# Kernel optimization log

Hardware: AMD Instinct MI355X
Metric: run time of the kernel (lower is better)

## Reference

```python
import jax, jax.numpy as jnp
import numpy as np

D_K = 64
D_MODEL = 1024
N_HEADS = 16


def setup_inputs() -> dict:
    key = jax.random.key(0)
    ks = jax.random.split(key, 9)
    B, S = 2, 2048
    scale = 1.0 / np.sqrt(D_MODEL)
    inp = {
        "x": jax.random.normal(ks[0], (B, S, D_MODEL), dtype=jnp.float32),
        "w_q": jax.random.normal(ks[1], (D_MODEL, N_HEADS * D_K), dtype=jnp.float32) * scale,
        "b_q": jnp.zeros((N_HEADS * D_K,), dtype=jnp.float32),
        "w_k": jax.random.normal(ks[2], (D_MODEL, N_HEADS * D_K), dtype=jnp.float32) * scale,
        "b_k": jnp.zeros((N_HEADS * D_K,), dtype=jnp.float32),
        "w_v": jax.random.normal(ks[3], (D_MODEL, N_HEADS * D_K), dtype=jnp.float32) * scale,
        "b_v": jnp.zeros((N_HEADS * D_K,), dtype=jnp.float32),
        "w_o": jax.random.normal(ks[4], (N_HEADS * D_K, D_MODEL), dtype=jnp.float32) * scale,
        "b_o": jnp.zeros((D_MODEL,), dtype=jnp.float32),
    }
    return inp


def reference(x, w_q, b_q, w_k, b_k, w_v, b_v, w_o, b_o):
    B, S, _ = x.shape
    H, Dk = N_HEADS, D_K

    def split_heads(m):  # [B,S,H*Dk] -> [B,H,S,Dk]
        return m.reshape(B, S, H, Dk).transpose(0, 2, 1, 3)

    Q = split_heads(x @ w_q + b_q)
    K = split_heads(x @ w_k + b_k)
    V = split_heads(x @ w_v + b_v)

    scores = jnp.einsum("bhsd,bhtd->bhst", Q, K) / jnp.sqrt(jnp.float32(Dk))
    probs = jax.nn.softmax(scores, axis=-1)
    attn = jnp.einsum("bhst,bhtd->bhsd", probs, V)  # [B,H,S,Dk]
    attn = attn.transpose(0, 2, 1, 3).reshape(B, S, H * Dk)
    return attn @ w_o + b_o
```

## Files before the change

### kernel.cpp

```cpp
#include <hip/hip_runtime.h>
#include <math.h>

#define D_MODELc 1024
#define N_HEADSc 16
#define D_Kc     64
#define B_SZc    2
#define S_LENc   2048
#define NTOKc    (B_SZc * S_LENc)

using half8  = __attribute__((ext_vector_type(8))) _Float16;
using half4  = __attribute__((ext_vector_type(4))) _Float16;
using fp16x2 = __attribute__((ext_vector_type(2))) __fp16;
using float4v = __attribute__((ext_vector_type(4))) float;

__global__ __launch_bounds__(256) void cvt_all(
    const float* __restrict__ x,
    const float* __restrict__ W0, const float* __restrict__ W1,
    const float* __restrict__ W2, const float* __restrict__ W3,
    _Float16* __restrict__ wout, _Float16* __restrict__ xout)
{
    __shared__ float T[32][33];
    const int z = blockIdx.z;
    const int t = threadIdx.x;

    if (z == 4) {
        const int bid = blockIdx.y * 32 + blockIdx.x;
        #pragma unroll
        for (int c = 0; c < 2; ++c) {
            const int i = bid * 512 + c * 256 + t;
            float4v a = ((const float4v*)x)[2 * i];
            float4v b = ((const float4v*)x)[2 * i + 1];
            half8 h;
            h[0] = (_Float16)a[0]; h[1] = (_Float16)a[1];
            h[2] = (_Float16)a[2]; h[3] = (_Float16)a[3];
            h[4] = (_Float16)b[0]; h[5] = (_Float16)b[1];
            h[6] = (_Float16)b[2]; h[7] = (_Float16)b[3];
            ((half8*)xout)[i] = h;
        }
        return;
    }

    const float* W = (z == 0) ? W0 : (z == 1) ? W1 : (z == 2) ? W2 : W3;
    _Float16* O = wout + (size_t)z * 1024 * 1024;

    const int k0 = blockIdx.x * 32;
    const int n0 = blockIdx.y * 32;
    {
        const int r = t >> 3, c4 = (t & 7) * 4;
        float4v v = *(const float4v*)(W + (size_t)(k0 + r) * 1024 + n0 + c4);
        T[r][c4 + 0] = v[0]; T[r][c4 + 1] = v[1];
        T[r][c4 + 2] = v[2]; T[r][c4 + 3] = v[3];
    }
    __syncthreads();
    {
        const int rn = t >> 3, ck4 = (t & 7) * 4;
        half4 h;
        h[0] = (_Float16)T[ck4 + 0][rn];
        h[1] = (_Float16)T[ck4 + 1][rn];
        h[2] = (_Float16)T[ck4 + 2][rn];
        h[3] = (_Float16)T[ck4 + 3][rn];
        *(half4*)(O + (size_t)(n0 + rn) * 1024 + k0 + ck4) = h;
    }
}

template <int MODE>
__global__ __launch_bounds__(256) void gemm_f16(
    const _Float16* __restrict__ A, const _Float16* __restrict__ BtAll,
    const float* __restrict__ bias0, const float* __restrict__ bias1,
    const float* __restrict__ bias2, void* __restrict__ Cout)
{
    __shared__ _Float16 Als[128 * 32];
    __shared__ _Float16 Bls[128 * 32];

    constexpr int K = 1024;
    const int tid = threadIdx.x;
    const int m0  = blockIdx.x * 128;
    const int n0  = blockIdx.y * 128;
    const int z   = blockIdx.z;

    const _Float16* Bt  = BtAll + (size_t)z * 1024 * 1024;
    const float* bias   = (z == 0) ? bias0 : (z == 1) ? bias1 : bias2;
    const float qscale  = (MODE == 1 && z == 0) ? 0.18033688011112042f : 1.0f;

    const int wave = tid >> 6, lane = tid & 63;
    const int wr = wave >> 1, wc = wave & 1;
    const int quad = lane >> 4, l16 = lane & 15;

    float4v acc[4][4];
    #pragma unroll
    for (int i = 0; i < 4; ++i)
        #pragma unroll
        for (int j = 0; j < 4; ++j)
            acc[i][j] = (float4v){0.f, 0.f, 0.f, 0.f};

    for (int k0 = 0; k0 < K; k0 += 32) {
        #pragma unroll
        for (int c = 0; c < 2; ++c) {
            const int i   = c * 256 + tid;
            const int row = i >> 2, kc = i & 3;
            const _Float16* ga = A  + (size_t)(m0 + row) * K + k0 + kc * 8;
            const _Float16* gb = Bt + (size_t)(n0 + row) * K + k0 + kc * 8;
            __builtin_amdgcn_global_load_lds(
                (const __attribute__((address_space(1))) void*)ga,
                (__attribute__((address_space(3))) void*)(Als + i * 8), 16, 0, 0);
            __builtin_amdgcn_global_load_lds(
                (const __attribute__((address_space(1))) void*)gb,
                (__attribute__((address_space(3))) void*)(Bls + i * 8), 16, 0, 0);
        }
        __syncthreads();

        half8 af[4], bf[4];
        #pragma unroll
        for (int i = 0; i < 4; ++i) {
            const int r = wr * 64 + i * 16 + l16;
            af[i] = *(const half8*)(Als + r * 32 + quad * 8);
        }
        #pragma unroll
        for (int j = 0; j < 4; ++j) {
            const int cidx = wc * 64 + j * 16 + l16;
            bf[j] = *(const half8*)(Bls + cidx * 32 + quad * 8);
        }
        #pragma unroll
        for (int i = 0; i < 4; ++i)
            #pragma unroll
            for (int j = 0; j < 4; ++j)
                acc[i][j] = __builtin_amdgcn_mfma_f32_16x16x32_f16(
                    af[i], bf[j], acc[i][j], 0, 0, 0);
        __syncthreads();
    }

    if constexpr (MODE == 0) {
        #pragma unroll
        for (int i = 0; i < 4; ++i) {
            const int rbase = m0 + wr * 64 + i * 16 + quad * 4;
            #pragma unroll
            for (int j = 0; j < 4; ++j) {
                const int col = n0 + wc * 64 + j * 16 + l16;
                const float bv = bias[col];
                #pragma unroll
                for (int r = 0; r < 4; ++r)
                    ((float*)Cout)[(size_t)(rbase + r) * 1024 + col] =
                        acc[i][j][r] + bv;
            }
        }
    } else {
        if (z != 2) {
            #pragma unroll
            for (int i = 0; i < 4; ++i) {
                const int rbase = m0 + wr * 64 + i * 16 + quad * 4;
                #pragma unroll
                for (int j = 0; j < 4; ++j) {
                    const int col = n0 + wc * 64 + j * 16 + l16;
                    const float bv = bias[col];
                    #pragma unroll
                    for (int r = 0; r < 4; ++r) {
                        const float v = (acc[i][j][r] + bv) * qscale;
                        const int n = rbase + r;
                        const int b = n >> 11, s = n & 2047;
                        const int h = col >> 6, d = col & 63;
                        _Float16* C = (_Float16*)Cout + (size_t)z * NTOKc * D_MODELc;
                        C[(((size_t)(b * N_HEADSc + h)) * S_LENc + s) * D_Kc + d] =
                            (_Float16)v;
                    }
                }
            }
        } else {
            #pragma unroll
            for (int i = 0; i < 4; ++i) {
                const int rbase = m0 + wr * 64 + i * 16 + quad * 4;
                const int b = rbase >> 11, s0 = rbase & 2047;
                #pragma unroll
                for (int j = 0; j < 4; ++j) {
                    const int col = n0 + wc * 64 + j * 16 + l16;
                    const float bv = bias[col];
                    const int h = col >> 6, d = col & 63;
                    half4 hv;
                    #pragma unroll
                    for (int r = 0; r < 4; ++r)
                        hv[r] = (_Float16)(acc[i][j][r] + bv);
                    _Float16* C = (_Float16*)Cout + (size_t)2 * NTOKc * D_MODELc;
                    *(half4*)(C + (((size_t)(b * N_HEADSc + h)) * D_Kc + d) *
                              S_LENc + s0) = hv;
                }
            }
        }
    }
}

__global__ __launch_bounds__(256) void attn_mfma(
    const _Float16* __restrict__ Qb, const _Float16* __restrict__ Kb,
    const _Float16* __restrict__ Vtg, _Float16* __restrict__ Op,
    float* __restrict__ Lp)
{
    constexpr int PS = 72;
    __shared__ _Float16 Ks[64 * PS];
    __shared__ _Float16 Vt[64 * PS];
    __shared__ _Float16 Ps[128 * PS];

    const int tid  = threadIdx.x;
    const int wv   = tid >> 6;
    const int lane = tid & 63;
    const int quad = lane >> 4;
    const int l16  = lane & 15;

    const int q0 = blockIdx.x * 128;
    const int bh = blockIdx.y;
    const int sp = blockIdx.z;
    const int kb = sp * (S_LENc / 2);

    const _Float16* Qsl = Qb  + (size_t)bh * S_LENc * D_Kc;
    const _Float16* Ksl = Kb  + (size_t)bh * S_LENc * D_Kc;
    const _Float16* Vsl = Vtg + (size_t)bh * S_LENc * D_Kc;

    half8 aq[2][2];
    #pragma unroll
    for (int qf = 0; qf < 2; ++qf) {
        const int row = q0 + wv * 32 + qf * 16 + l16;
        aq[qf][0] = *(const half8*)(Qsl + (size_t)row * 64 + quad * 8);
        aq[qf][1] = *(const half8*)(Qsl + (size_t)row * 64 + 32 + quad * 8);
    }

    float4v O[2][4];
    #pragma unroll
    for (int qf = 0; qf < 2; ++qf)
        #pragma unroll
        for (int nt = 0; nt < 4; ++nt)
            O[qf][nt] = (float4v){0.f, 0.f, 0.f, 0.f};
    float lr[2] = {0.f, 0.f};

    const int sr = tid >> 2;
    const int sg = (tid & 3) * 16;

    for (int t0 = kb; t0 < kb + S_LENc / 2; t0 += 64) {
        half8 k0 = *(const half8*)(Ksl + (size_t)(t0 + sr) * 64 + sg);
        half8 k1 = *(const half8*)(Ksl + (size_t)(t0 + sr) * 64 + sg + 8);
        half8 v0 = *(const half8*)(Vsl + (size_t)sr * S_LENc + t0 + sg);
        half8 v1 = *(const half8*)(Vsl + (size_t)sr * S_LENc + t0 + sg + 8);
        __syncthreads();
        *(half8*)(Ks + sr * PS + sg)     = k0;
        *(half8*)(Ks + sr * PS + sg + 8) = k1;
        *(half8*)(Vt + sr * PS + sg)     = v0;
        *(half8*)(Vt + sr * PS + sg + 8) = v1;
        __syncthreads();

        half8 kf[4][2];
        #pragma unroll
        for (int nt = 0; nt < 4; ++nt) {
            kf[nt][0] = *(const half8*)(Ks + (nt * 16 + l16) * PS + quad * 8);
            kf[nt][1] = *(const half8*)(Ks + (nt * 16 + l16) * PS + 32 + quad * 8);
        }

        #pragma unroll
        for (int qf = 0; qf < 2; ++qf) {
            float4v st[4];
            #pragma unroll
            for (int nt = 0; nt < 4; ++nt) {
                st[nt] = __builtin_amdgcn_mfma_f32_16x16x32_f16(
                    kf[nt][0], aq[qf][0], (float4v){0.f, 0.f, 0.f, 0.f}, 0, 0, 0);
                st[nt] = __builtin_amdgcn_mfma_f32_16x16x32_f16(
                    kf[nt][1], aq[qf][1], st[nt], 0, 0, 0);
            }
            float ls = 0.f;
            #pragma unroll
            for (int nt = 0; nt < 4; ++nt) {
                const float p0 = __builtin_amdgcn_exp2f(fminf(st[nt][0], 15.5f));
                const float p1 = __builtin_amdgcn_exp2f(fminf(st[nt][1], 15.5f));
                const float p2 = __builtin_amdgcn_exp2f(fminf(st[nt][2], 15.5f));
                const float p3 = __builtin_amdgcn_exp2f(fminf(st[nt][3], 15.5f));
                ls += (p0 + p1) + (p2 + p3);
                union { fp16x2 h2[2]; half4 h4; } u;
                u.h2[0] = __builtin_amdgcn_cvt_pkrtz(p0, p1);
                u.h2[1] = __builtin_amdgcn_cvt_pkrtz(p2, p3);
                *(half4*)(Ps + (wv * 32 + qf * 16 + l16) * PS +
                          nt * 16 + quad * 4) = u.h4;
            }
            lr[qf] += ls;
        }

        half8 bvv[4][2];
        #pragma unroll
        for (int nt = 0; nt < 4; ++nt) {
            bvv[nt][0] = *(const half8*)(Vt + (nt * 16 + l16) * PS + quad * 8);
            bvv[nt][1] = *(const half8*)(Vt + (nt * 16 + l16) * PS + 32 + quad * 8);
        }
        #pragma unroll
        for (int qf = 0; qf < 2; ++qf) {
            half8 ap0 = *(const half8*)(Ps + (wv * 32 + qf * 16 + l16) * PS + quad * 8);
            half8 ap1 = *(const half8*)(Ps + (wv * 32 + qf * 16 + l16) * PS + 32 + quad * 8);
            #pragma unroll
            for (int nt = 0; nt < 4; ++nt) {
                O[qf][nt] = __builtin_amdgcn_mfma_f32_16x16x32_f16(
                    ap0, bvv[nt][0], O[qf][nt], 0, 0, 0);
                O[qf][nt] = __builtin_amdgcn_mfma_f32_16x16x32_f16(
                    ap1, bvv[nt][1], O[qf][nt], 0, 0, 0);
            }
        }
    }

    const size_t qgb = (size_t)bh * S_LENc;
    #pragma unroll
    for (int qf = 0; qf < 2; ++qf) {
        float t = lr[qf];
        t += __shfl_xor(t, 16, 64);
        t += __shfl_xor(t, 32, 64);
        if (quad == 0)
            Lp[(size_t)sp * 65536 + qgb + q0 + wv * 32 + qf * 16 + l16] = t;
        #pragma unroll
        for (int r = 0; r < 4; ++r) {
            const int q = q0 + wv * 32 + qf * 16 + quad * 4 + r;
            _Float16* dst = Op + ((size_t)sp * 65536 + qgb + q) * 64;
            #pragma unroll
            for (int nt = 0; nt < 4; ++nt)
                dst[nt * 16 + l16] = (_Float16)O[qf][nt][r];
        }
    }
}

__global__ __launch_bounds__(256) void attn_combine(
    const _Float16* __restrict__ Op, const float* __restrict__ Lp,
    _Float16* __restrict__ Ab)
{
    const int i  = blockIdx.x * 256 + threadIdx.x;
    const int e0 = i * 8;
    const int qg = e0 >> 6;
    const int d0 = e0 & 63;
    const int bh = qg >> 11, q = qg & 2047;
    const int b  = bh >> 4,  h = bh & 15;

    const float inv = 1.0f / (Lp[qg] + Lp[65536 + qg]);
    half8 o0 = *(const half8*)(Op + (size_t)qg * 64 + d0);
    half8 o1 = *(const half8*)(Op + ((size_t)65536 + qg) * 64 + d0);
    half8 hv;
    #pragma unroll
    for (int j = 0; j < 8; ++j)
        hv[j] = (_Float16)(((float)o0[j] + (float)o1[j]) * inv);
    *(half8*)(Ab + ((size_t)(b * S_LENc + q)) * 1024 + h * 64 + d0) = hv;
}

extern "C" void kernel_launch(void* const* d_in, const int* in_sizes, int n_in,
                              void* d_out, int out_size, void* d_ws, size_t ws_size,
                              hipStream_t stream)
{
    const float* x  = (const float*)d_in[0];
    const float* wq = (const float*)d_in[1];
    const float* bq = (const float*)d_in[2];
    const float* wk = (const float*)d_in[3];
    const float* bk = (const float*)d_in[4];
    const float* wv = (const float*)d_in[5];
    const float* bv = (const float*)d_in[6];
    const float* wo = (const float*)d_in[7];
    const float* bo = (const float*)d_in[8];
    float* out = (float*)d_out;

    const size_t M1 = 1024 * 1024;
    const size_t M4 = 4 * M1;
    _Float16* xh = (_Float16*)d_ws;
    _Float16* wh = xh + M4;
    _Float16* Qh = wh + M4;
    _Float16* Oph = Qh + 3 * M4;
    float*    Lp  = (float*)(Oph + 2 * M4);
    _Float16* Ah = xh;

    cvt_all<<<dim3(32, 32, 5), dim3(256), 0, stream>>>(
        x, wq, wk, wv, wo, wh, xh);
    gemm_f16<1><<<dim3(NTOKc / 128, D_MODELc / 128, 3), dim3(256), 0, stream>>>(
        xh, wh, bq, bk, bv, Qh);
    attn_mfma<<<dim3(S_LENc / 128, B_SZc * N_HEADSc, 2), dim3(256), 0, stream>>>(
        Qh, Qh + M4, Qh + 2 * M4, Oph, Lp);
    attn_combine<<<dim3(NTOKc * D_MODELc / 8 / 256), dim3(256), 0, stream>>>(
        Oph, Lp, Ah);
    gemm_f16<0><<<dim3(NTOKc / 128, D_MODELc / 128, 1), dim3(256), 0, stream>>>(
        Ah, wh + 3 * M1, bo, bo, bo, out);
}
```

Before: 218.9 us.

## Prefetch next K/V tile in attention and use smaller output GEMM tiles

The attention loop now loads the next K/V tile from global memory into registers while the current tile is processed, so global latency overlaps with MFMA work. The output projection gets its own kernel with 64x128 tiles, doubling the block count from 256 to 512 to better fill the GPU's compute units. The QKV GEMM is split out as a non-template kernel. Risks are higher register pressure in attention, an extra wasted prefetch on the last iteration, and less reuse per block in the output GEMM.

```diff
diff --git a/kernel.cpp b/kernel.cpp
--- a/kernel.cpp
+++ b/kernel.cpp
@@ -63,11 +63,10 @@
     }
 }
 
-template <int MODE>
-__global__ __launch_bounds__(256) void gemm_f16(
+__global__ __launch_bounds__(256) void gemm_qkv(
     const _Float16* __restrict__ A, const _Float16* __restrict__ BtAll,
     const float* __restrict__ bias0, const float* __restrict__ bias1,
-    const float* __restrict__ bias2, void* __restrict__ Cout)
+    const float* __restrict__ bias2, _Float16* __restrict__ Cout)
 {
     __shared__ _Float16 Als[128 * 32];
     __shared__ _Float16 Bls[128 * 32];
@@ -80,7 +79,7 @@
 
     const _Float16* Bt  = BtAll + (size_t)z * 1024 * 1024;
     const float* bias   = (z == 0) ? bias0 : (z == 1) ? bias1 : bias2;
-    const float qscale  = (MODE == 1 && z == 0) ? 0.18033688011112042f : 1.0f;
+    const float qscale  = (z == 0) ? 0.18033688011112042f : 1.0f;
 
     const int wave = tid >> 6, lane = tid & 63;
     const int wr = wave >> 1, wc = wave & 1;
@@ -111,15 +110,11 @@
 
         half8 af[4], bf[4];
         #pragma unroll
-        for (int i = 0; i < 4; ++i) {
-            const int r = wr * 64 + i * 16 + l16;
-            af[i] = *(const half8*)(Als + r * 32 + quad * 8);
-        }
-        #pragma unroll
-        for (int j = 0; j < 4; ++j) {
-            const int cidx = wc * 64 + j * 16 + l16;
-            bf[j] = *(const half8*)(Bls + cidx * 32 + quad * 8);
-        }
+        for (int i = 0; i < 4; ++i)
+            af[i] = *(const half8*)(Als + (wr * 64 + i * 16 + l16) * 32 + quad * 8);
+        #pragma unroll
+        for (int j = 0; j < 4; ++j)
+            bf[j] = *(const half8*)(Bls + (wc * 64 + j * 16 + l16) * 32 + quad * 8);
         #pragma unroll
         for (int i = 0; i < 4; ++i)
             #pragma unroll
@@ -129,7 +124,7 @@
         __syncthreads();
     }
 
-    if constexpr (MODE == 0) {
+    if (z != 2) {
         #pragma unroll
         for (int i = 0; i < 4; ++i) {
             const int rbase = m0 + wr * 64 + i * 16 + quad * 4;
@@ -138,51 +133,107 @@
                 const int col = n0 + wc * 64 + j * 16 + l16;
                 const float bv = bias[col];
                 #pragma unroll
-                for (int r = 0; r < 4; ++r)
-                    ((float*)Cout)[(size_t)(rbase + r) * 1024 + col] =
-                        acc[i][j][r] + bv;
-            }
-        }
-    } else {
-        if (z != 2) {
-            #pragma unroll
-            for (int i = 0; i < 4; ++i) {
-                const int rbase = m0 + wr * 64 + i * 16 + quad * 4;
-                #pragma unroll
-                for (int j = 0; j < 4; ++j) {
-                    const int col = n0 + wc * 64 + j * 16 + l16;
-                    const float bv = bias[col];
-                    #pragma unroll
-                    for (int r = 0; r < 4; ++r) {
-                        const float v = (acc[i][j][r] + bv) * qscale;
-                        const int n = rbase + r;
-                        const int b = n >> 11, s = n & 2047;
-                        const int h = col >> 6, d = col & 63;
-                        _Float16* C = (_Float16*)Cout + (size_t)z * NTOKc * D_MODELc;
-                        C[(((size_t)(b * N_HEADSc + h)) * S_LENc + s) * D_Kc + d] =
-                            (_Float16)v;
-                    }
+                for (int r = 0; r < 4; ++r) {
+                    const float v = (acc[i][j][r] + bv) * qscale;
+                    const int n = rbase + r;
+                    const int b = n >> 11, s = n & 2047;
+                    const int h = col >> 6, d = col & 63;
+                    _Float16* C = Cout + (size_t)z * NTOKc * D_MODELc;
+                    C[(((size_t)(b * N_HEADSc + h)) * S_LENc + s) * D_Kc + d] =
+                        (_Float16)v;
                 }
             }
-        } else {
-            #pragma unroll
-            for (int i = 0; i < 4; ++i) {
-                const int rbase = m0 + wr * 64 + i * 16 + quad * 4;
-                const int b = rbase >> 11, s0 = rbase & 2047;
+        }
+    } else {
+        #pragma unroll
+        for (int i = 0; i < 4; ++i) {
+            const int rbase = m0 + wr * 64 + i * 16 + quad * 4;
+            const int b = rbase >> 11, s0 = rbase & 2047;
+            #pragma unroll
+            for (int j = 0; j < 4; ++j) {
+                const int col = n0 + wc * 64 + j * 16 + l16;
+                const float bv = bias[col];
+                const int h = col >> 6, d = col & 63;
+                half4 hv;
                 #pragma unroll
-                for (int j = 0; j < 4; ++j) {
-                    const int col = n0 + wc * 64 + j * 16 + l16;
-                    const float bv = bias[col];
-                    const int h = col >> 6, d = col & 63;
-                    half4 hv;
-                    #pragma unroll
-                    for (int r = 0; r < 4; ++r)
-                        hv[r] = (_Float16)(acc[i][j][r] + bv);
-                    _Float16* C = (_Float16*)Cout + (size_t)2 * NTOKc * D_MODELc;
-                    *(half4*)(C + (((size_t)(b * N_HEADSc + h)) * D_Kc + d) *
-                              S_LENc + s0) = hv;
-                }
+                for (int r = 0; r < 4; ++r)
+                    hv[r] = (_Float16)(acc[i][j][r] + bv);
+                _Float16* C = Cout + (size_t)2 * NTOKc * D_MODELc;
+                *(half4*)(C + (((size_t)(b * N_HEADSc + h)) * D_Kc + d) *
+                          S_LENc + s0) = hv;
             }
+        }
+    }
+}
+
+__global__ __launch_bounds__(256) void gemm_out(
+    const _Float16* __restrict__ A, const _Float16* __restrict__ Bt,
+    const float* __restrict__ bias, float* __restrict__ C)
+{
+    __shared__ _Float16 Als[64 * 32];
+    __shared__ _Float16 Bls[128 * 32];
+
+    constexpr int K = 1024;
+    const int tid = threadIdx.x;
+    const int m0  = blockIdx.x * 64;
+    const int n0  = blockIdx.y * 128;
+
+    const int wave = tid >> 6, lane = tid & 63;
+    const int wr = wave >> 1, wc = wave & 1;
+    const int quad = lane >> 4, l16 = lane & 15;
+
+    float4v acc[2][4];
+    #pragma unroll
+    for (int i = 0; i < 2; ++i)
+        #pragma unroll
+        for (int j = 0; j < 4; ++j)
+            acc[i][j] = (float4v){0.f, 0.f, 0.f, 0.f};
+
+    for (int k0 = 0; k0 < K; k0 += 32) {
+        {
+            const int row = tid >> 2, kc = tid & 3;
+            __builtin_amdgcn_global_load_lds(
+                (const __attribute__((address_space(1))) void*)
+                    (A + (size_t)(m0 + row) * K + k0 + kc * 8),
+                (__attribute__((address_space(3))) void*)(Als + tid * 8), 16, 0, 0);
+        }
+        #pragma unroll
+        for (int c = 0; c < 2; ++c) {
+            const int i = c * 256 + tid;
+            const int row = i >> 2, kc = i & 3;
+            __builtin_amdgcn_global_load_lds(
+                (const __attribute__((address_space(1))) void*)
+                    (Bt + (size_t)(n0 + row) * K + k0 + kc * 8),
+                (__attribute__((address_space(3))) void*)(Bls + i * 8), 16, 0, 0);
+        }
+        __syncthreads();
+
+        half8 af[2], bf[4];
+        #pragma unroll
+        for (int i = 0; i < 2; ++i)
+            af[i] = *(const half8*)(Als + (wr * 32 + i * 16 + l16) * 32 + quad * 8);
+        #pragma unroll
+        for (int j = 0; j < 4; ++j)
+            bf[j] = *(const half8*)(Bls + (wc * 64 + j * 16 + l16) * 32 + quad * 8);
+        #pragma unroll
+        for (int i = 0; i < 2; ++i)
+            #pragma unroll
+            for (int j = 0; j < 4; ++j)
+                acc[i][j] = __builtin_amdgcn_mfma_f32_16x16x32_f16(
+                    af[i], bf[j], acc[i][j], 0, 0, 0);
+        __syncthreads();
+    }
+
+    #pragma unroll
+    for (int i = 0; i < 2; ++i) {
+        const int rbase = m0 + wr * 32 + i * 16 + quad * 4;
+        #pragma unroll
+        for (int j = 0; j < 4; ++j) {
+            const int col = n0 + wc * 64 + j * 16 + l16;
+            const float bv = bias[col];
+            #pragma unroll
+            for (int r = 0; r < 4; ++r)
+                C[(size_t)(rbase + r) * 1024 + col] = acc[i][j][r] + bv;
         }
     }
 }
@@ -207,6 +258,7 @@
     const int bh = blockIdx.y;
     const int sp = blockIdx.z;
     const int kb = sp * (S_LENc / 2);
+    const int kend = kb + S_LENc / 2;
 
     const _Float16* Qsl = Qb  + (size_t)bh * S_LENc * D_Kc;
     const _Float16* Ksl = Kb  + (size_t)bh * S_LENc * D_Kc;
@@ -231,17 +283,24 @@
     const int sr = tid >> 2;
     const int sg = (tid & 3) * 16;
 
-    for (int t0 = kb; t0 < kb + S_LENc / 2; t0 += 64) {
-        half8 k0 = *(const half8*)(Ksl + (size_t)(t0 + sr) * 64 + sg);
-        half8 k1 = *(const half8*)(Ksl + (size_t)(t0 + sr) * 64 + sg + 8);
-        half8 v0 = *(const half8*)(Vsl + (size_t)sr * S_LENc + t0 + sg);
-        half8 v1 = *(const half8*)(Vsl + (size_t)sr * S_LENc + t0 + sg + 8);
+    half8 k0 = *(const half8*)(Ksl + (size_t)(kb + sr) * 64 + sg);
+    half8 k1 = *(const half8*)(Ksl + (size_t)(kb + sr) * 64 + sg + 8);
+    half8 v0 = *(const half8*)(Vsl + (size_t)sr * S_LENc + kb + sg);
+    half8 v1 = *(const half8*)(Vsl + (size_t)sr * S_LENc + kb + sg + 8);
+
+    for (int t0 = kb; t0 < kend; t0 += 64) {
         __syncthreads();
         *(half8*)(Ks + sr * PS + sg)     = k0;
         *(half8*)(Ks + sr * PS + sg + 8) = k1;
         *(half8*)(Vt + sr * PS + sg)     = v0;
         *(half8*)(Vt + sr * PS + sg + 8) = v1;
         __syncthreads();
+
+        const int tn = (t0 + 64 < kend) ? t0 + 64 : kb;
+        k0 = *(const half8*)(Ksl + (size_t)(tn + sr) * 64 + sg);
+        k1 = *(const half8*)(Ksl + (size_t)(tn + sr) * 64 + sg + 8);
+        v0 = *(const half8*)(Vsl + (size_t)sr * S_LENc + tn + sg);
+        v1 = *(const half8*)(Vsl + (size_t)sr * S_LENc + tn + sg + 8);
 
         half8 kf[4][2];
         #pragma unroll
@@ -363,12 +422,12 @@
 
     cvt_all<<<dim3(32, 32, 5), dim3(256), 0, stream>>>(
         x, wq, wk, wv, wo, wh, xh);
-    gemm_f16<1><<<dim3(NTOKc / 128, D_MODELc / 128, 3), dim3(256), 0, stream>>>(
+    gemm_qkv<<<dim3(NTOKc / 128, D_MODELc / 128, 3), dim3(256), 0, stream>>>(
         xh, wh, bq, bk, bv, Qh);
     attn_mfma<<<dim3(S_LENc / 128, B_SZc * N_HEADSc, 2), dim3(256), 0, stream>>>(
         Qh, Qh + M4, Qh + 2 * M4, Oph, Lp);
     attn_combine<<<dim3(NTOKc * D_MODELc / 8 / 256), dim3(256), 0, stream>>>(
         Oph, Lp, Ah);
-    gemm_f16<0><<<dim3(NTOKc / 128, D_MODELc / 128, 1), dim3(256), 0, stream>>>(
-        Ah, wh + 3 * M1, bo, bo, bo, out);
-}
+    gemm_out<<<dim3(NTOKc / 64, D_MODELc / 128), dim3(256), 0, stream>>>(
+        Ah, wh + 3 * M1, bo, out);
+}
```

Measured after the change: 217.5 us. Within noise of the previous version (-0.7%).
